# Performance work log

Hardware: AMD Instinct MI355X
Metric: run time of the kernel (lower is better)

The kernel has to match this reference:

```python
import jax, jax.numpy as jnp
import numpy as np

B = 65536  # number of 32-bit words processed by the VM


def _build_tables():
    # ByteToNibbleFFN: byte one-hot -> (high, low) nibble one-hots
    W1_b2n = np.eye(256, dtype=np.float32)
    W2_b2n = np.zeros((256, 32), dtype=np.float32)
    for b in range(256):
        W2_b2n[b, (b >> 4) & 15] = 1.0
        W2_b2n[b, 16 + (b & 15)] = 1.0
    # NibbleToByteFFN: (high, low) -> byte one-hot
    W1_n2b = np.zeros((32, 256), dtype=np.float32)
    for high in range(16):
        for low in range(16):
            bv = (high << 4) | low
            W1_n2b[high, bv] = 1.0
            W1_n2b[16 + low, bv] = 1.0
    W2_n2b = np.eye(256, dtype=np.float32)
    # NibbleTableFFN for XOR
    W1_xor = np.zeros((32, 256), dtype=np.float32)
    W2_xor = np.zeros((256, 16), dtype=np.float32)
    for a in range(16):
        for b in range(16):
            k = a * 16 + b
            W1_xor[a, k] = 1.0
            W1_xor[16 + b, k] = 1.0
            W2_xor[k, (a ^ b) & 15] = 1.0
    # NibbleAddFFN: (a, b, carry) -> (sum, carry)
    W1_add = np.zeros((34, 512), dtype=np.float32)
    W2_sum = np.zeros((512, 16), dtype=np.float32)
    W2_carry = np.zeros((512, 2), dtype=np.float32)
    for a in range(16):
        for b in range(16):
            for c in range(2):
                k = a * 32 + b * 2 + c
                W1_add[a, k] = 1.0
                W1_add[16 + b, k] = 1.0
                W1_add[32 + c, k] = 1.0
                total = a + b + c
                W2_sum[k, total & 15] = 1.0
                W2_carry[k, 1 if total >= 16 else 0] = 1.0
    return (jnp.asarray(W1_b2n), jnp.asarray(W2_b2n), jnp.asarray(W1_n2b),
            jnp.asarray(W2_n2b), jnp.asarray(W1_xor), jnp.asarray(W2_xor),
            jnp.asarray(W1_add), jnp.asarray(W2_sum), jnp.asarray(W2_carry))


def setup_inputs() -> dict:
    key = jax.random.key(0)
    k1, k2 = jax.random.split(key)
    a_idx = jax.random.randint(k1, (B, 4), 0, 256)
    b_idx = jax.random.randint(k2, (B, 4), 0, 256)
    a_bytes = jax.nn.one_hot(a_idx, 256, dtype=jnp.float32)  # [B,4,256]
    b_bytes = jax.nn.one_hot(b_idx, 256, dtype=jnp.float32)
    (W1_b2n, W2_b2n, W1_n2b, W2_n2b, W1_xor, W2_xor,
     W1_add, W2_sum, W2_carry) = _build_tables()
    return {
        'a_bytes': a_bytes, 'b_bytes': b_bytes,
        'W1_b2n': W1_b2n, 'W2_b2n': W2_b2n,
        'W1_n2b': W1_n2b, 'W2_n2b': W2_n2b,
        'W1_xor': W1_xor, 'W2_xor': W2_xor,
        'W1_add': W1_add, 'W2_sum': W2_sum, 'W2_carry': W2_carry,
    }


def reference(a_bytes, b_bytes, W1_b2n, W2_b2n, W1_n2b, W2_n2b,
              W1_xor, W2_xor, W1_add, W2_sum, W2_carry):
    # Batched faithful translation of the torch VM: the torch code loops over
    # single words; here each op is vectorized over the word batch B while the
    # fixed 4-byte carry chain remains an explicit (structural) loop.
    def byte_to_nib(x):                       # x: [B,256]
        w = jax.nn.softmax((x @ W1_b2n) * 100.0, axis=-1)
        nib = w @ W2_b2n                      # [B,32]
        return nib[:, :16], nib[:, 16:]

    def nib_to_byte(high, low):               # [B,16] each -> [B,256]
        x = jnp.concatenate([high, low], axis=-1)
        w = jax.nn.softmax((x @ W1_n2b - 1.5) * 20.0, axis=-1)
        return w @ W2_n2b

    def nib_xor(a, b):                        # [B,16] each -> [B,16]
        x = jnp.concatenate([a, b], axis=-1)
        w = jax.nn.softmax((x @ W1_xor - 1.5) * 20.0, axis=-1)
        return w @ W2_xor

    def nib_add(a, b, c):                     # [B,16],[B,16],[B,2]
        x = jnp.concatenate([a, b, c], axis=-1)
        w = jax.nn.softmax((x @ W1_add - 2.5) * 20.0, axis=-1)
        return w @ W2_sum, w @ W2_carry

    def byte_xor(a, b):                       # [B,256] each
        a_h, a_l = byte_to_nib(a)
        b_h, b_l = byte_to_nib(b)
        return nib_to_byte(nib_xor(a_h, b_h), nib_xor(a_l, b_l))

    n = a_bytes.shape[0]
    # ByteAddFFN: 4-byte ripple-carry add, carry starts as one-hot 0
    carry = jnp.broadcast_to(jnp.array([1.0, 0.0], dtype=a_bytes.dtype), (n, 2))
    sum_bytes = []
    for i in range(4):
        a_h, a_l = byte_to_nib(a_bytes[:, i])
        b_h, b_l = byte_to_nib(b_bytes[:, i])
        r_low, carry_low = nib_add(a_l, b_l, carry)
        r_high, carry = nib_add(a_h, b_h, carry_low)
        sum_bytes.append(nib_to_byte(r_high, r_low))
    # Chain a second VM op: XOR the sum with operand a, per byte
    out = [byte_xor(sum_bytes[i], a_bytes[:, i]) for i in range(4)]
    return jnp.stack(out, axis=1)             # [B,4,256]
```

## Files before the change

kernel.cpp:

```cpp
#include <hip/hip_runtime.h>
#include <stdint.h>

__global__ __launch_bounds__(256) void vm_kernel(
    const float* __restrict__ a_bytes,
    const float* __restrict__ b_bytes,
    float* __restrict__ out)
{
    const int word     = blockIdx.x;
    const int t        = threadIdx.x;
    const int byte_pos = t >> 6;
    const int lane     = t & 63;
    const long base = (long)word * 1024 + byte_pos * 256 + lane * 4;

    const float4 av = *(const float4*)(a_bytes + base);
    const float4 bv = *(const float4*)(b_bytes + base);

    const float j0 = (float)(lane * 4);
    float pa = av.x * j0 + av.y * (j0 + 1.0f) + av.z * (j0 + 2.0f) + av.w * (j0 + 3.0f);
    float pb = bv.x * j0 + bv.y * (j0 + 1.0f) + bv.z * (j0 + 2.0f) + bv.w * (j0 + 3.0f);
#pragma unroll
    for (int off = 32; off >= 1; off >>= 1) {
        pa += __shfl_xor(pa, off, 64);
        pb += __shfl_xor(pb, off, 64);
    }

    __shared__ int a_idx[4];
    __shared__ int b_idx[4];
    __shared__ int out_idx[4];
    if (lane == 0) {
        a_idx[byte_pos] = (int)(pa + 0.5f);
        b_idx[byte_pos] = (int)(pb + 0.5f);
    }
    __syncthreads();
    if (t == 0) {
        uint32_t aw = (uint32_t)a_idx[0] | ((uint32_t)a_idx[1] << 8) |
                      ((uint32_t)a_idx[2] << 16) | ((uint32_t)a_idx[3] << 24);
        uint32_t bw = (uint32_t)b_idx[0] | ((uint32_t)b_idx[1] << 8) |
                      ((uint32_t)b_idx[2] << 16) | ((uint32_t)b_idx[3] << 24);
        uint32_t s = aw + bw;
        uint32_t o = s ^ aw;
        out_idx[0] = (int)(o & 255u);
        out_idx[1] = (int)((o >> 8) & 255u);
        out_idx[2] = (int)((o >> 16) & 255u);
        out_idx[3] = (int)((o >> 24) & 255u);
    }
    __syncthreads();

    const int oi = out_idx[byte_pos];
    const int j  = lane * 4;
    float4 ov;
    ov.x = (j     == oi) ? 1.0f : 0.0f;
    ov.y = (j + 1 == oi) ? 1.0f : 0.0f;
    ov.z = (j + 2 == oi) ? 1.0f : 0.0f;
    ov.w = (j + 3 == oi) ? 1.0f : 0.0f;
    *(float4*)(out + base) = ov;
}

extern "C" void kernel_launch(void* const* d_in, const int* in_sizes, int n_in,
                              void* d_out, int out_size, void* d_ws, size_t ws_size,
                              hipStream_t stream)
{
    const float* a_bytes = (const float*)d_in[0];
    const float* b_bytes = (const float*)d_in[1];
    float* out = (float*)d_out;
    const int n_words = in_sizes[0] / 1024;
    vm_kernel<<<n_words, 256, 0, stream>>>(a_bytes, b_bytes, out);
}
```

Measured before the change: 581.6 us.

## Process one word per wave with ballot decode and grid-stride loop

Assigns each 64-lane wave a whole 32-bit word, loading all four bytes of both operands per lane. The one-hot index is decoded with wave ballots and find-first-set instead of shuffle reductions, so shared memory and block barriers are no longer needed. Launches a fixed 2048-block persistent grid with a grid-stride loop and uses nontemporal stores for the output. The ballot decode assumes exactly one element above 0.5 per byte, which holds for clean one-hot inputs.

```diff
diff --git a/kernel.cpp b/kernel.cpp
--- a/kernel.cpp
+++ b/kernel.cpp
@@ -1,59 +1,64 @@
 #include <hip/hip_runtime.h>
 #include <stdint.h>
 
-__global__ __launch_bounds__(256) void vm_kernel(
+typedef float f32x4 __attribute__((ext_vector_type(4)));
+
+__global__ __launch_bounds__(256, 8) void vm_kernel(
     const float* __restrict__ a_bytes,
     const float* __restrict__ b_bytes,
-    float* __restrict__ out)
+    float* __restrict__ out,
+    int n_words)
 {
-    const int word     = blockIdx.x;
-    const int t        = threadIdx.x;
-    const int byte_pos = t >> 6;
-    const int lane     = t & 63;
-    const long base = (long)word * 1024 + byte_pos * 256 + lane * 4;
+    const int lane   = threadIdx.x & 63;
+    const int wave   = blockIdx.x * (blockDim.x >> 6) + (threadIdx.x >> 6);
+    const int nwaves = gridDim.x * (blockDim.x >> 6);
 
-    const float4 av = *(const float4*)(a_bytes + base);
-    const float4 bv = *(const float4*)(b_bytes + base);
+    for (int w = wave; w < n_words; w += nwaves) {
+        const long base = (long)w * 1024 + lane * 4;
+        const float* pa = a_bytes + base;
+        const float* pb = b_bytes + base;
 
-    const float j0 = (float)(lane * 4);
-    float pa = av.x * j0 + av.y * (j0 + 1.0f) + av.z * (j0 + 2.0f) + av.w * (j0 + 3.0f);
-    float pb = bv.x * j0 + bv.y * (j0 + 1.0f) + bv.z * (j0 + 2.0f) + bv.w * (j0 + 3.0f);
+        const f32x4 a0 = *(const f32x4*)(pa);
+        const f32x4 a1 = *(const f32x4*)(pa + 256);
+        const f32x4 a2 = *(const f32x4*)(pa + 512);
+        const f32x4 a3 = *(const f32x4*)(pa + 768);
+        const f32x4 b0 = *(const f32x4*)(pb);
+        const f32x4 b1 = *(const f32x4*)(pb + 256);
+        const f32x4 b2 = *(const f32x4*)(pb + 512);
+        const f32x4 b3 = *(const f32x4*)(pb + 768);
+
+        auto idx_of = [&](const f32x4 v) -> uint32_t {
+            const uint64_t m0 = __ballot(v.x > 0.5f);
+            const uint64_t m1 = __ballot(v.y > 0.5f);
+            const uint64_t m2 = __ballot(v.z > 0.5f);
+            const uint64_t m3 = __ballot(v.w > 0.5f);
+            const uint64_t m  = m0 | m1 | m2 | m3;
+            const uint32_t hl = (uint32_t)__ffsll((unsigned long long)m) - 1u;
+            const uint32_t c  = (m1 ? 1u : 0u) | (m2 ? 2u : 0u) | (m3 ? 3u : 0u);
+            return hl * 4u + c;
+        };
+
+        const uint32_t aw = idx_of(a0) | (idx_of(a1) << 8) |
+                            (idx_of(a2) << 16) | (idx_of(a3) << 24);
+        const uint32_t bw = idx_of(b0) | (idx_of(b1) << 8) |
+                            (idx_of(b2) << 16) | (idx_of(b3) << 24);
+
+        const uint32_t s = aw + bw;
+        const uint32_t o = s ^ aw;
+
+        float* po = out + base;
+        const int j = lane * 4;
 #pragma unroll
-    for (int off = 32; off >= 1; off >>= 1) {
-        pa += __shfl_xor(pa, off, 64);
-        pb += __shfl_xor(pb, off, 64);
+        for (int k = 0; k < 4; ++k) {
+            const int oi = (int)((o >> (8 * k)) & 255u);
+            f32x4 ov;
+            ov.x = (j     == oi) ? 1.0f : 0.0f;
+            ov.y = (j + 1 == oi) ? 1.0f : 0.0f;
+            ov.z = (j + 2 == oi) ? 1.0f : 0.0f;
+            ov.w = (j + 3 == oi) ? 1.0f : 0.0f;
+            __builtin_nontemporal_store(ov, (f32x4*)(po + k * 256));
+        }
     }
-
-    __shared__ int a_idx[4];
-    __shared__ int b_idx[4];
-    __shared__ int out_idx[4];
-    if (lane == 0) {
-        a_idx[byte_pos] = (int)(pa + 0.5f);
-        b_idx[byte_pos] = (int)(pb + 0.5f);
-    }
-    __syncthreads();
-    if (t == 0) {
-        uint32_t aw = (uint32_t)a_idx[0] | ((uint32_t)a_idx[1] << 8) |
-                      ((uint32_t)a_idx[2] << 16) | ((uint32_t)a_idx[3] << 24);
-        uint32_t bw = (uint32_t)b_idx[0] | ((uint32_t)b_idx[1] << 8) |
-                      ((uint32_t)b_idx[2] << 16) | ((uint32_t)b_idx[3] << 24);
-        uint32_t s = aw + bw;
-        uint32_t o = s ^ aw;
-        out_idx[0] = (int)(o & 255u);
-        out_idx[1] = (int)((o >> 8) & 255u);
-        out_idx[2] = (int)((o >> 16) & 255u);
-        out_idx[3] = (int)((o >> 24) & 255u);
-    }
-    __syncthreads();
-
-    const int oi = out_idx[byte_pos];
-    const int j  = lane * 4;
-    float4 ov;
-    ov.x = (j     == oi) ? 1.0f : 0.0f;
-    ov.y = (j + 1 == oi) ? 1.0f : 0.0f;
-    ov.z = (j + 2 == oi) ? 1.0f : 0.0f;
-    ov.w = (j + 3 == oi) ? 1.0f : 0.0f;
-    *(float4*)(out + base) = ov;
 }
 
 extern "C" void kernel_launch(void* const* d_in, const int* in_sizes, int n_in,
@@ -64,5 +69,7 @@
     const float* b_bytes = (const float*)d_in[1];
     float* out = (float*)d_out;
     const int n_words = in_sizes[0] / 1024;
-    vm_kernel<<<n_words, 256, 0, stream>>>(a_bytes, b_bytes, out);
+
+    const int blocks = 2048;
+    vm_kernel<<<blocks, 256, 0, stream>>>(a_bytes, b_bytes, out, n_words);
 }
```

New measurement: 604.3 us. +3.9%, slower.
